# Optimization experiments

Hardware: AMD Instinct MI355X
Metric: run time of the kernel (lower is better)

The kernel has to match this reference:

```python
import jax, jax.numpy as jnp
import numpy as np

CHUNK = 64  # rows of A processed per step; bounds the [CHUNK,K,N] intermediate


def setup_inputs() -> dict:
    key = jax.random.key(0)
    k1, k2, k3 = jax.random.split(key, 3)
    in_features, out_features = 768, 768
    x = jax.random.normal(k1, (2, 1024, in_features), dtype=jnp.float32)
    # kaiming_uniform_(a=sqrt(5)) on [out,in] -> bound = 1/sqrt(in_features)
    wb = 1.0 / np.sqrt(in_features)
    weight = jax.random.uniform(k2, (out_features, in_features), minval=-wb, maxval=wb, dtype=jnp.float32)
    bias = jax.random.uniform(k3, (out_features,), minval=-wb, maxval=wb, dtype=jnp.float32)
    return {"x": x, "weight": weight, "bias": bias}


def _mam(A, B):
    # A: [M, K], B: [K, N]. C[i,j] = max_k A[i,k]*B[k,j] + min_k A[i,k]*B[k,j]
    M, K = A.shape
    N = B.shape[1]
    def chunk_fn(a):  # a: [CHUNK, K]
        p = a[:, :, None] * B[None, :, :]  # [CHUNK, K, N]
        return jnp.max(p, axis=1) + jnp.min(p, axis=1)
    n_chunks = M // CHUNK
    C = jax.lax.map(chunk_fn, A.reshape(n_chunks, CHUNK, K))  # [n_chunks, CHUNK, N]
    return C.reshape(M, N)


def reference(x, weight, bias):
    # beta = 0 path: pure MAM + bias (matches MAMDense.forward with beta=False)
    K = x.shape[-1]
    x_flat = x.reshape(-1, K)               # [M, K]
    C = _mam(x_flat, weight.T)              # [M, N]
    C = C + bias[None, :]
    return C.reshape(x.shape[:-1] + (weight.shape[0],))
```

## Files before the change

### kernel.cpp

```cpp
#include <hip/hip_runtime.h>
#include <math.h>


#define M_DIM 2048
#define N_DIM 768
#define K_DIM 768

#define BM 64
#define BN 32
#define BK 64
#define KP (BK / 2)
#define NTILES (K_DIM / BK)

#define SA (2 * BM + 4)
#define SB (2 * BN + 4)

typedef __attribute__((ext_vector_type(4))) float f32x4;

__device__ __forceinline__ float max3f(float a, float b, float c) {
    float d;
    asm("v_max3_f32 %0, %1, %2, %3" : "=v"(d) : "v"(a), "v"(b), "v"(c));
    return d;
}
__device__ __forceinline__ float min3f(float a, float b, float c) {
    float d;
    asm("v_min3_f32 %0, %1, %2, %3" : "=v"(d) : "v"(a), "v"(b), "v"(c));
    return d;
}

__global__ __launch_bounds__(256, 3) void mam_kernel(
    const float* __restrict__ A, const float* __restrict__ W,
    const float* __restrict__ bias, float* __restrict__ out)
{
    __shared__ __align__(16) float As[KP * SA];
    __shared__ __align__(16) float Bs[KP * SB];

    const int tid = threadIdx.x;
    const int m0 = blockIdx.y * BM;
    const int n0 = blockIdx.x * BN;
    const int mt = tid >> 4;
    const int nt = tid & 15;

    float amax[4][2], amin[4][2];
#pragma unroll
    for (int i = 0; i < 4; ++i)
#pragma unroll
        for (int j = 0; j < 2; ++j) {
            amax[i][j] = -INFINITY;
            amin[i][j] =  INFINITY;
        }

    const int ar  = tid >> 2;
    const int aks = tid & 3;
    const int br  = tid >> 3;
    const int bks = tid & 7;

    const float* Ap = A + (size_t)(m0 + ar) * K_DIM + aks * 16;
    const float* Wp = W + (size_t)(n0 + br) * K_DIM + bks * 8;

    const float bb0 = bias[n0 + nt * 2 + 0];
    const float bb1 = bias[n0 + nt * 2 + 1];

    float* aw = &As[(aks * 8) * SA + 2 * ar];
    float* bw = &Bs[(bks * 4) * SB + 2 * br];
    const float* Ard = &As[(mt * 4) * 2];
    const float* Brd = &Bs[(nt * 2) * 2];

    float4 pa[4], pb[2];
#pragma unroll
    for (int q = 0; q < 4; ++q) pa[q] = *(const float4*)(Ap + 4 * q);
#pragma unroll
    for (int q = 0; q < 2; ++q) pb[q] = *(const float4*)(Wp + 4 * q);

    for (int kt = 0; kt < NTILES; ++kt) {
        if (kt) __syncthreads();

#pragma unroll
        for (int q = 0; q < 4; ++q) {
            *(float2*)(aw + (2 * q + 0) * SA) = make_float2(pa[q].x, pa[q].y);
            *(float2*)(aw + (2 * q + 1) * SA) = make_float2(pa[q].z, pa[q].w);
        }
#pragma unroll
        for (int q = 0; q < 2; ++q) {
            *(float2*)(bw + (2 * q + 0) * SB) = make_float2(pb[q].x, pb[q].y);
            *(float2*)(bw + (2 * q + 1) * SB) = make_float2(pb[q].z, pb[q].w);
        }
        __syncthreads();

        if (kt + 1 < NTILES) {
            const float* An = Ap + (kt + 1) * BK;
            const float* Wn = Wp + (kt + 1) * BK;
#pragma unroll
            for (int q = 0; q < 4; ++q) pa[q] = *(const float4*)(An + 4 * q);
#pragma unroll
            for (int q = 0; q < 2; ++q) pb[q] = *(const float4*)(Wn + 4 * q);
        }

#pragma unroll
        for (int kk2 = 0; kk2 < KP; ++kk2) {
            const f32x4 a01 = *(const f32x4*)(Ard + kk2 * SA);
            const f32x4 a23 = *(const f32x4*)(Ard + kk2 * SA + 4);
            const f32x4 b01 = *(const f32x4*)(Brd + kk2 * SB);
            const float am[4][2] = {{a01.x, a01.y}, {a01.z, a01.w},
                                    {a23.x, a23.y}, {a23.z, a23.w}};
            const float bn_[2][2] = {{b01.x, b01.y}, {b01.z, b01.w}};
#pragma unroll
            for (int i = 0; i < 4; ++i)
#pragma unroll
                for (int j = 0; j < 2; ++j) {
                    const float p0 = am[i][0] * bn_[j][0];
                    const float p1 = am[i][1] * bn_[j][1];
                    amax[i][j] = max3f(amax[i][j], p0, p1);
                    amin[i][j] = min3f(amin[i][j], p0, p1);
                }
        }
    }

#pragma unroll
    for (int i = 0; i < 4; ++i) {
        float2 o;
        o.x = amax[i][0] + amin[i][0] + bb0;
        o.y = amax[i][1] + amin[i][1] + bb1;
        *(float2*)&out[(size_t)(m0 + mt * 4 + i) * N_DIM + n0 + nt * 2] = o;
    }
}

extern "C" void kernel_launch(void* const* d_in, const int* in_sizes, int n_in,
                              void* d_out, int out_size, void* d_ws, size_t ws_size,
                              hipStream_t stream) {
    const float* x    = (const float*)d_in[0];
    const float* w    = (const float*)d_in[1];
    const float* bias = (const float*)d_in[2];
    float* out = (float*)d_out;

    dim3 grid(N_DIM / BN, M_DIM / BM);
    mam_kernel<<<grid, 256, 0, stream>>>(x, w, bias, out);
}
```

Before: 74.81 us.

## Switch MAM inner loop to packed fp16 products with max/min accumulation

```diff
diff --git a/kernel.cpp b/kernel.cpp
--- a/kernel.cpp
+++ b/kernel.cpp
@@ -12,28 +12,22 @@
 #define KP (BK / 2)
 #define NTILES (K_DIM / BK)
 
-#define SA (2 * BM + 4)
-#define SB (2 * BN + 4)
+#define SAH 66
+#define SBH 34
 
-typedef __attribute__((ext_vector_type(4))) float f32x4;
+typedef _Float16 h2 __attribute__((ext_vector_type(2)));
+typedef _Float16 h4 __attribute__((ext_vector_type(4)));
 
-__device__ __forceinline__ float max3f(float a, float b, float c) {
-    float d;
-    asm("v_max3_f32 %0, %1, %2, %3" : "=v"(d) : "v"(a), "v"(b), "v"(c));
-    return d;
-}
-__device__ __forceinline__ float min3f(float a, float b, float c) {
-    float d;
-    asm("v_min3_f32 %0, %1, %2, %3" : "=v"(d) : "v"(a), "v"(b), "v"(c));
-    return d;
+__device__ __forceinline__ h2 cvt_pk(float x, float y) {
+    return __builtin_bit_cast(h2, __builtin_amdgcn_cvt_pkrtz(x, y));
 }
 
 __global__ __launch_bounds__(256, 3) void mam_kernel(
     const float* __restrict__ A, const float* __restrict__ W,
     const float* __restrict__ bias, float* __restrict__ out)
 {
-    __shared__ __align__(16) float As[KP * SA];
-    __shared__ __align__(16) float Bs[KP * SB];
+    __shared__ __align__(16) h2 As[KP * SAH];
+    __shared__ __align__(16) h2 Bs[KP * SBH];
 
     const int tid = threadIdx.x;
     const int m0 = blockIdx.y * BM;
@@ -41,49 +35,49 @@
     const int mt = tid >> 4;
     const int nt = tid & 15;
 
-    float amax[4][2], amin[4][2];
+    h2 pmax[4][2], pmin[4][2];
+    const _Float16 HMIN = (_Float16)(-65504.0f), HMAX = (_Float16)(65504.0f);
 #pragma unroll
     for (int i = 0; i < 4; ++i)
 #pragma unroll
         for (int j = 0; j < 2; ++j) {
-            amax[i][j] = -INFINITY;
-            amin[i][j] =  INFINITY;
+            pmax[i][j] = (h2){HMIN, HMIN};
+            pmin[i][j] = (h2){HMAX, HMAX};
         }
 
-    const int ar  = tid >> 2;
-    const int aks = tid & 3;
-    const int br  = tid >> 3;
-    const int bks = tid & 7;
-
-    const float* Ap = A + (size_t)(m0 + ar) * K_DIM + aks * 16;
-    const float* Wp = W + (size_t)(n0 + br) * K_DIM + bks * 8;
+    const int arow = tid >> 4;
+    const int akc  = tid & 15;
+    const float* Ap = A + (size_t)m0 * K_DIM + akc * 4;
+    const float* Wp = W + (size_t)n0 * K_DIM + akc * 4;
 
     const float bb0 = bias[n0 + nt * 2 + 0];
     const float bb1 = bias[n0 + nt * 2 + 1];
 
-    float* aw = &As[(aks * 8) * SA + 2 * ar];
-    float* bw = &Bs[(bks * 4) * SB + 2 * br];
-    const float* Ard = &As[(mt * 4) * 2];
-    const float* Brd = &Bs[(nt * 2) * 2];
+    h2* awr = &As[2 * akc * SAH];
+    h2* bwr = &Bs[2 * akc * SBH];
+    const h2* Ard = &As[mt * 4];
+    const h2* Brd = &Bs[nt * 2];
 
     float4 pa[4], pb[2];
 #pragma unroll
-    for (int q = 0; q < 4; ++q) pa[q] = *(const float4*)(Ap + 4 * q);
+    for (int q = 0; q < 4; ++q)
+        pa[q] = *(const float4*)(Ap + (size_t)(arow + 16 * q) * K_DIM);
 #pragma unroll
-    for (int q = 0; q < 2; ++q) pb[q] = *(const float4*)(Wp + 4 * q);
+    for (int q = 0; q < 2; ++q)
+        pb[q] = *(const float4*)(Wp + (size_t)(arow + 16 * q) * K_DIM);
 
     for (int kt = 0; kt < NTILES; ++kt) {
         if (kt) __syncthreads();
 
 #pragma unroll
         for (int q = 0; q < 4; ++q) {
-            *(float2*)(aw + (2 * q + 0) * SA) = make_float2(pa[q].x, pa[q].y);
-            *(float2*)(aw + (2 * q + 1) * SA) = make_float2(pa[q].z, pa[q].w);
+            awr[0 * SAH + arow + 16 * q] = cvt_pk(pa[q].x, pa[q].y);
+            awr[1 * SAH + arow + 16 * q] = cvt_pk(pa[q].z, pa[q].w);
         }
 #pragma unroll
         for (int q = 0; q < 2; ++q) {
-            *(float2*)(bw + (2 * q + 0) * SB) = make_float2(pb[q].x, pb[q].y);
-            *(float2*)(bw + (2 * q + 1) * SB) = make_float2(pb[q].z, pb[q].w);
+            bwr[0 * SBH + arow + 16 * q] = cvt_pk(pb[q].x, pb[q].y);
+            bwr[1 * SBH + arow + 16 * q] = cvt_pk(pb[q].z, pb[q].w);
         }
         __syncthreads();
 
@@ -91,27 +85,27 @@
             const float* An = Ap + (kt + 1) * BK;
             const float* Wn = Wp + (kt + 1) * BK;
 #pragma unroll
-            for (int q = 0; q < 4; ++q) pa[q] = *(const float4*)(An + 4 * q);
+            for (int q = 0; q < 4; ++q)
+                pa[q] = *(const float4*)(An + (size_t)(arow + 16 * q) * K_DIM);
 #pragma unroll
-            for (int q = 0; q < 2; ++q) pb[q] = *(const float4*)(Wn + 4 * q);
+            for (int q = 0; q < 2; ++q)
+                pb[q] = *(const float4*)(Wn + (size_t)(arow + 16 * q) * K_DIM);
         }
 
 #pragma unroll
         for (int kk2 = 0; kk2 < KP; ++kk2) {
-            const f32x4 a01 = *(const f32x4*)(Ard + kk2 * SA);
-            const f32x4 a23 = *(const f32x4*)(Ard + kk2 * SA + 4);
-            const f32x4 b01 = *(const f32x4*)(Brd + kk2 * SB);
-            const float am[4][2] = {{a01.x, a01.y}, {a01.z, a01.w},
-                                    {a23.x, a23.y}, {a23.z, a23.w}};
-            const float bn_[2][2] = {{b01.x, b01.y}, {b01.z, b01.w}};
+            const h4 a01 = *(const h4*)(Ard + kk2 * SAH);
+            const h4 a23 = *(const h4*)(Ard + kk2 * SAH + 2);
+            const h4 b01 = *(const h4*)(Brd + kk2 * SBH);
+            const h2 am[4] = {a01.xy, a01.zw, a23.xy, a23.zw};
+            const h2 bn[2] = {b01.xy, b01.zw};
 #pragma unroll
             for (int i = 0; i < 4; ++i)
 #pragma unroll
                 for (int j = 0; j < 2; ++j) {
-                    const float p0 = am[i][0] * bn_[j][0];
-                    const float p1 = am[i][1] * bn_[j][1];
-                    amax[i][j] = max3f(amax[i][j], p0, p1);
-                    amin[i][j] = min3f(amin[i][j], p0, p1);
+                    const h2 p = am[i] * bn[j];
+                    pmax[i][j] = __builtin_elementwise_max(pmax[i][j], p);
+                    pmin[i][j] = __builtin_elementwise_min(pmin[i][j], p);
                 }
         }
     }
@@ -119,8 +113,10 @@
 #pragma unroll
     for (int i = 0; i < 4; ++i) {
         float2 o;
-        o.x = amax[i][0] + amin[i][0] + bb0;
-        o.y = amax[i][1] + amin[i][1] + bb1;
+        o.x = fmaxf((float)pmax[i][0].x, (float)pmax[i][0].y)
+            + fminf((float)pmin[i][0].x, (float)pmin[i][0].y) + bb0;
+        o.y = fmaxf((float)pmax[i][1].x, (float)pmax[i][1].y)
+            + fminf((float)pmin[i][1].x, (float)pmin[i][1].y) + bb1;
         *(float2*)&out[(size_t)(m0 + mt * 4 + i) * N_DIM + n0 + nt * 2] = o;
     }
 }
```

New measurement: 68.85 us. 8.0% less time.
